# Kernel optimization log

Measured on AMD Instinct MI355X. Metric: run time of the kernel, lower is better.

Reference implementation:

```python
import jax, jax.numpy as jnp
from jax import lax
import numpy as np

B, T, I, H, L, O = 256, 200, 32, 512, 2, 7
EPS = 1e-12


def setup_inputs() -> dict:
    key = jax.random.key(0)
    ks = jax.random.split(key, 11)
    s = 0.05
    return {
        "x": jax.random.normal(ks[0], (B, T, I), dtype=jnp.float32),
        "w_ih0": jax.random.normal(ks[1], (4 * H, I), dtype=jnp.float32) * s,
        "w_hh0": jax.random.normal(ks[2], (4 * H, H), dtype=jnp.float32) * s,
        "b_ih0": jax.random.normal(ks[3], (4 * H,), dtype=jnp.float32) * s,
        "b_hh0": jax.random.normal(ks[4], (4 * H,), dtype=jnp.float32) * s,
        "w_ih1": jax.random.normal(ks[5], (4 * H, H), dtype=jnp.float32) * s,
        "w_hh1": jax.random.normal(ks[6], (4 * H, H), dtype=jnp.float32) * s,
        "b_ih1": jax.random.normal(ks[7], (4 * H,), dtype=jnp.float32) * s,
        "b_hh1": jax.random.normal(ks[8], (4 * H,), dtype=jnp.float32) * s,
        "w_fc": jax.random.normal(ks[9], (O, H), dtype=jnp.float32) * s,
        "b_fc": jax.random.normal(ks[10], (O,), dtype=jnp.float32) * s,
    }


def _lstm_layer(x_tbi, w_ih, w_hh, b_ih, b_hh):
    # x_tbi: [T, B, in]; PyTorch gate order i, f, g, o
    b = b_ih + b_hh
    hdim = w_hh.shape[1]
    batch = x_tbi.shape[1]
    # precompute input projections for all timesteps (one big GEMM)
    xg = jnp.einsum('tbi,gi->tbg', x_tbi, w_ih) + b  # [T, B, 4H]

    def step(carry, xgt):
        h, c = carry
        g = xgt + h @ w_hh.T
        i, f, gg, o = jnp.split(g, 4, axis=-1)
        c = jax.nn.sigmoid(f) * c + jax.nn.sigmoid(i) * jnp.tanh(gg)
        h = jax.nn.sigmoid(o) * jnp.tanh(c)
        return (h, c), h

    h0 = jnp.zeros((batch, hdim), x_tbi.dtype)
    (_, _), hs = lax.scan(step, (h0, h0), xg)
    return hs  # [T, B, H]


def reference(x, w_ih0, w_hh0, b_ih0, b_hh0, w_ih1, w_hh1, b_ih1, b_hh1, w_fc, b_fc):
    xt = jnp.transpose(x, (1, 0, 2))  # [T, B, I]
    h1 = _lstm_layer(xt, w_ih0, w_hh0, b_ih0, b_hh0)
    h2 = _lstm_layer(h1, w_ih1, w_hh1, b_ih1, b_hh1)
    last = h2[-1]  # [B, H] = output[:, -1, :]
    y = last @ w_fc.T + b_fc  # [B, O]
    p = jax.nn.sigmoid(y[:, :3])
    rt = jnp.tanh(y[:, 3:])
    # F.normalize(p=2, dim=1, eps=1e-12)
    r = rt / jnp.maximum(jnp.linalg.norm(rt, axis=1, keepdims=True), EPS)
    return (p, r)
```

## Files before the change

### kernel.cpp

```cpp
#include <hip/hip_runtime.h>
#include <hip/hip_bf16.h>

#define TSEQ  200
#define BATCH 256
#define INDIM 32
#define HID   512
#define GATES 2048

typedef __bf16 bf16x8 __attribute__((ext_vector_type(8)));
typedef float  f32x4  __attribute__((ext_vector_type(4)));
typedef unsigned long long u64;

static constexpr size_t OFF_PW_IH0 = 0;
static constexpr size_t OFF_PW_HH0 = 0x20000;
static constexpr size_t OFF_PW_IH1 = 0x220000;
static constexpr size_t OFF_PW_HH1 = 0x420000;
static constexpr size_t OFF_B0     = 0x620000;
static constexpr size_t OFF_B1     = 0x622000;
static constexpr size_t OFF_H1     = 0x624000;
static constexpr size_t OFF_H2     = 0x724000;
static constexpr size_t OFF_CTR    = 0x7A4000;
static constexpr size_t OFF_H2P    = 0x7A6000;
static constexpr size_t ZERO_OFF   = OFF_H1;
static constexpr size_t ZERO_LEN   = OFF_H2P + 0x80000 - OFF_H1;

__device__ __forceinline__ float sigm(float v) { return 1.f / (1.f + __expf(-v)); }

__device__ __forceinline__ bf16x8 as_bf16x8(f32x4 v) {
    union { f32x4 f; bf16x8 b; } u; u.f = v; return u.b;
}

__device__ __forceinline__ bf16x8 load16_coh(const bf16x8* p) {
    bf16x8 v;
    asm volatile("global_load_dwordx4 %0, %1, off sc0 sc1"
                 : "=v"(v) : "v"(p) : "memory");
    return v;
}

__device__ __forceinline__ void store16_coh(void* p, u64 v0, u64 v1) {
    union { u64 u[2]; f32x4 f; } cv; cv.u[0] = v0; cv.u[1] = v1;
    asm volatile("global_store_dwordx4 %0, %1, off sc0 sc1"
                 :: "v"(p), "v"(cv.f) : "memory");
}

__device__ __forceinline__ unsigned load_flag_coh(const unsigned* p) {
    unsigned v;
    asm volatile("global_load_dword %0, %1, off sc0 sc1\n\t"
                 "s_waitcnt vmcnt(0)"
                 : "=v"(v) : "v"(p) : "memory");
    return v;
}

__global__ void pack_w(const float* __restrict__ W, __bf16* __restrict__ out, int ktlog2)
{
    int tid = blockIdx.x * 256 + threadIdx.x;
    int K = 32 << ktlog2;
    int j    = tid & 7;
    int lane = (tid >> 3) & 63;
    int rest = tid >> 9;
    int kt   = rest & ((1 << ktlog2) - 1);
    int r2   = rest >> ktlog2;
    int lnt  = r2 & 7;
    int bn   = r2 >> 3;
    int type = lnt >> 1, half = lnt & 1;
    int g    = type * 512 + bn * 32 + half * 16 + (lane & 15);
    int kcol = kt * 32 + (lane >> 4) * 8 + j;
    out[tid] = (__bf16)W[g * K + kcol];
}

__global__ void bias_comb(const float* __restrict__ a0, const float* __restrict__ a1,
                          const float* __restrict__ a2, const float* __restrict__ a3,
                          float* __restrict__ o0, float* __restrict__ o1)
{
    int tid = blockIdx.x * 256 + threadIdx.x;
    if (tid < GATES) { o0[tid] = a0[tid] + a1[tid]; o1[tid] = a2[tid] + a3[tid]; }
}

__global__ __launch_bounds__(256, 1) void lstm_persist(const float* __restrict__ x,
                                                       const float* __restrict__ wfc,
                                                       const float* __restrict__ bfc,
                                                       char* __restrict__ ws,
                                                       float* __restrict__ out)
{
    const int layer = blockIdx.x >> 7;
    const int lb    = blockIdx.x & 127;
    const int mtp   = lb >> 4;
    const int bn    = lb & 15;
    const int wid   = threadIdx.x >> 6;
    const int half  = wid & 1;
    const int kh    = wid >> 1;
    const int lane  = threadIdx.x & 63;
    const int q     = lane >> 4;
    const int c16   = lane & 15;
    unsigned* flg   = (unsigned*)(ws + OFF_CTR) + (size_t)mtp * 64;

    __shared__ float  red[2][64][33];
    __shared__ __bf16 htr[1024];

    const float* bias = (const float*)(ws + (layer ? OFF_B1 : OFF_B0));
    const int hidx = bn * 32 + half * 16 + c16;
    const float bi  = bias[hidx];
    const float bff = bias[512 + hidx];
    const float bg  = bias[1024 + hidx];
    const float bo  = bias[1536 + hidx];

    const bf16x8* __restrict__ pBx = (const bf16x8*)(ws + OFF_PW_IH0);
    const bf16x8* __restrict__ pBh = (const bf16x8*)(ws + OFF_PW_HH0);
    const bf16x8* __restrict__ pB1 = (const bf16x8*)(ws + OFF_PW_IH1);
    const bf16x8* __restrict__ pB2 = (const bf16x8*)(ws + OFF_PW_HH1);
    float* __restrict__ h2p = (float*)(ws + OFF_H2P);

    f32x4 Bw[64];
    f32x4 Bx[4];
    if (layer == 0) {
        #pragma unroll
        for (int j = 0; j < 8; ++j)
            #pragma unroll
            for (int ty = 0; ty < 4; ++ty)
                Bw[j * 4 + ty] = *(const f32x4*)&pBh[((bn * 8 + ty * 2 + half) * 16 + kh * 8 + j) * 64 + lane];
        #pragma unroll
        for (int ty = 0; ty < 4; ++ty)
            Bx[ty] = *(const f32x4*)&pBx[(bn * 8 + ty * 2 + half) * 64 + lane];
    } else {
        const bf16x8* __restrict__ pW = kh ? pB2 : pB1;
        #pragma unroll
        for (int j = 0; j < 16; ++j)
            #pragma unroll
            for (int ty = 0; ty < 4; ++ty)
                Bw[j * 4 + ty] = *(const f32x4*)&pW[((bn * 8 + ty * 2 + half) * 16 + j) * 64 + lane];
    }

    float creg[8] = {0.f,0.f,0.f,0.f,0.f,0.f,0.f,0.f};

    auto loadA = [&](bf16x8* dst, const bf16x8* pA, int kt0) {
        #pragma unroll
        for (int j = 0; j < 8; ++j) {
            dst[j]     = load16_coh(&pA[((mtp * 2 + 0) * 16 + kt0 + j) * 64 + lane]);
            dst[8 + j] = load16_coh(&pA[((mtp * 2 + 1) * 16 + kt0 + j) * 64 + lane]);
        }
    };

    for (int k = 0; k <= TSEQ; ++k) {
        const bool active = layer ? (k >= 1) : (k < TSEQ);
        if (active) {
            const int t = k - layer;
            f32x4 acc[2][4] = {};

            const size_t h1rd = OFF_H1 + (size_t)((k + 3) & 3) * 0x40000;

            if (layer == 0) {
                const bf16x8* __restrict__ pA = (const bf16x8*)(ws + h1rd);
                bf16x8 af[16];
                loadA(af, pA, kh * 8);
                bf16x8 ax[2];
                if (kh == 0) {
                    #pragma unroll
                    for (int m = 0; m < 2; ++m) {
                        const int b = (mtp * 2 + m) * 16 + c16;
                        const float* xp = x + ((size_t)b * TSEQ + t) * INDIM + q * 8;
                        float4 xlo = *(const float4*)xp;
                        float4 xhi = *(const float4*)(xp + 4);
                        ax[m][0] = (__bf16)xlo.x; ax[m][1] = (__bf16)xlo.y;
                        ax[m][2] = (__bf16)xlo.z; ax[m][3] = (__bf16)xlo.w;
                        ax[m][4] = (__bf16)xhi.x; ax[m][5] = (__bf16)xhi.y;
                        ax[m][6] = (__bf16)xhi.z; ax[m][7] = (__bf16)xhi.w;
                    }
                }
                asm volatile("s_waitcnt vmcnt(0)" ::: "memory");
                __builtin_amdgcn_sched_barrier(0);
                if (kh == 0) {
                    #pragma unroll
                    for (int m = 0; m < 2; ++m)
                        #pragma unroll
                        for (int ty = 0; ty < 4; ++ty)
                            acc[m][ty] = __builtin_amdgcn_mfma_f32_16x16x32_bf16(ax[m], as_bf16x8(Bx[ty]), acc[m][ty], 0, 0, 0);
                }
                #pragma unroll
                for (int j = 0; j < 8; ++j) {
                    #pragma unroll
                    for (int ty = 0; ty < 4; ++ty) {
                        acc[0][ty] = __builtin_amdgcn_mfma_f32_16x16x32_bf16(af[j],     as_bf16x8(Bw[j * 4 + ty]), acc[0][ty], 0, 0, 0);
                        acc[1][ty] = __builtin_amdgcn_mfma_f32_16x16x32_bf16(af[8 + j], as_bf16x8(Bw[j * 4 + ty]), acc[1][ty], 0, 0, 0);
                    }
                }
            } else {
                const bf16x8* __restrict__ pA = kh
                    ? (const bf16x8*)(ws + OFF_H2 + (size_t)((k + 1) & 1) * 0x40000)
                    : (const bf16x8*)(ws + h1rd);
                bf16x8 a0[16], a1[16];
                loadA(a0, pA, 0);
                loadA(a1, pA, 8);
                asm volatile("s_waitcnt vmcnt(0)" ::: "memory");
                __builtin_amdgcn_sched_barrier(0);
                #pragma unroll
                for (int j = 0; j < 8; ++j) {
                    #pragma unroll
                    for (int ty = 0; ty < 4; ++ty) {
                        acc[0][ty] = __builtin_amdgcn_mfma_f32_16x16x32_bf16(a0[j],     as_bf16x8(Bw[j * 4 + ty]), acc[0][ty], 0, 0, 0);
                        acc[1][ty] = __builtin_amdgcn_mfma_f32_16x16x32_bf16(a0[8 + j], as_bf16x8(Bw[j * 4 + ty]), acc[1][ty], 0, 0, 0);
                    }
                }
                #pragma unroll
                for (int j = 0; j < 8; ++j) {
                    #pragma unroll
                    for (int ty = 0; ty < 4; ++ty) {
                        acc[0][ty] = __builtin_amdgcn_mfma_f32_16x16x32_bf16(a1[j],     as_bf16x8(Bw[(8 + j) * 4 + ty]), acc[0][ty], 0, 0, 0);
                        acc[1][ty] = __builtin_amdgcn_mfma_f32_16x16x32_bf16(a1[8 + j], as_bf16x8(Bw[(8 + j) * 4 + ty]), acc[1][ty], 0, 0, 0);
                    }
                }
            }

            if (kh == 1) {
                #pragma unroll
                for (int m = 0; m < 2; ++m)
                    #pragma unroll
                    for (int ty = 0; ty < 4; ++ty)
                        #pragma unroll
                        for (int r = 0; r < 4; ++r)
                            red[half][lane][m * 16 + ty * 4 + r] = acc[m][ty][r];
            }
            __syncthreads();

            if (kh == 0) {
                __bf16* __restrict__ hout = (__bf16*)(ws + (layer
                    ? OFF_H2 + (size_t)(k & 1) * 0x40000
                    : OFF_H1 + (size_t)(k & 3) * 0x40000));
                #pragma unroll
                for (int m = 0; m < 2; ++m) {
                    #pragma unroll
                    for (int r = 0; r < 4; ++r) {
                        float pi = acc[m][0][r] + red[half][lane][m * 16 + r]      + bi;
                        float pf = acc[m][1][r] + red[half][lane][m * 16 + 4 + r]  + bff;
                        float pg = acc[m][2][r] + red[half][lane][m * 16 + 8 + r]  + bg;
                        float po = acc[m][3][r] + red[half][lane][m * 16 + 12 + r] + bo;
                        float cn = sigm(pf) * creg[m * 4 + r] + sigm(pi) * tanhf(pg);
                        float hn = sigm(po) * tanhf(cn);
                        creg[m * 4 + r] = cn;
                        htr[half * 512 + (m * 16 + q * 4 + r) * 16 + c16] = (__bf16)hn;
                        if (layer == 1 && k == TSEQ) {
                            const int b = (mtp * 2 + m) * 16 + q * 4 + r;
                            __hip_atomic_store(&h2p[b * HID + hidx], hn,
                                               __ATOMIC_RELAXED, __HIP_MEMORY_SCOPE_AGENT);
                        }
                    }
                }
                const int bt   = lane >> 5;
                const int qa1  = (lane >> 4) & 1;
                const int b15r = lane & 15;
                const u64* lp = (const u64*)&htr[half * 512 + (bt * 16 + b15r) * 16 + qa1 * 8];
                u64 v0 = lp[0], v1 = lp[1];
                const int f = (((mtp * 2 + bt) * 16) + bn) * 64 + (half * 2 + qa1) * 16 + b15r;
                u64* gp = (u64*)hout + (size_t)f * 2;
                store16_coh(gp, v0, v1);
            }
        }

        asm volatile("s_waitcnt vmcnt(0)" ::: "memory");
        __syncthreads();
        if (threadIdx.x == 0)
            __hip_atomic_store(flg + layer * 16 + bn, (unsigned)(k + 1),
                               __ATOMIC_RELAXED, __HIP_MEMORY_SCOPE_AGENT);
        if (threadIdx.x < 32) {
            const int need = (layer == 0 && threadIdx.x >= 16 && k < TSEQ) ? (k - 1) : (k + 1);
            while ((int)load_flag_coh(flg + threadIdx.x) < need)
                __builtin_amdgcn_s_sleep(1);
        }
        __syncthreads();
    }

    if (threadIdx.x < 64) {
        const int b = mtp * 32 + layer * 16 + bn;
        const float* h = h2p + b * HID;
        float hv[8];
        #pragma unroll
        for (int j = 0; j < 8; ++j)
            hv[j] = __hip_atomic_load(&h[lane * 8 + j], __ATOMIC_RELAXED, __HIP_MEMORY_SCOPE_AGENT);
        float y[7];
        #pragma unroll
        for (int o = 0; o < 7; ++o) {
            const float* wrow = wfc + o * HID;
            float s = 0.f;
            #pragma unroll
            for (int j = 0; j < 8; ++j) s += hv[j] * wrow[lane * 8 + j];
            #pragma unroll
            for (int off = 32; off >= 1; off >>= 1) s += __shfl_down(s, off);
            y[o] = s;
        }
        if (lane == 0) {
            out[b * 3 + 0] = sigm(y[0] + bfc[0]);
            out[b * 3 + 1] = sigm(y[1] + bfc[1]);
            out[b * 3 + 2] = sigm(y[2] + bfc[2]);
            float r0 = tanhf(y[3] + bfc[3]);
            float r1 = tanhf(y[4] + bfc[4]);
            float r2 = tanhf(y[5] + bfc[5]);
            float r3 = tanhf(y[6] + bfc[6]);
            float n = sqrtf(r0 * r0 + r1 * r1 + r2 * r2 + r3 * r3);
            n = fmaxf(n, 1e-12f);
            out[768 + b * 4 + 0] = r0 / n;
            out[768 + b * 4 + 1] = r1 / n;
            out[768 + b * 4 + 2] = r2 / n;
            out[768 + b * 4 + 3] = r3 / n;
        }
    }
}

extern "C" void kernel_launch(void* const* d_in, const int* in_sizes, int n_in,
                              void* d_out, int out_size, void* d_ws, size_t ws_size,
                              hipStream_t stream)
{
    const float* x    = (const float*)d_in[0];
    const float* wih0 = (const float*)d_in[1];
    const float* whh0 = (const float*)d_in[2];
    const float* bih0 = (const float*)d_in[3];
    const float* bhh0 = (const float*)d_in[4];
    const float* wih1 = (const float*)d_in[5];
    const float* whh1 = (const float*)d_in[6];
    const float* bih1 = (const float*)d_in[7];
    const float* bhh1 = (const float*)d_in[8];
    const float* wfc  = (const float*)d_in[9];
    const float* bfc  = (const float*)d_in[10];
    char* ws = (char*)d_ws;

    hipMemsetAsync(ws + ZERO_OFF, 0, ZERO_LEN, stream);

    pack_w<<<256,  256, 0, stream>>>(wih0, (__bf16*)(ws + OFF_PW_IH0), 0);
    pack_w<<<4096, 256, 0, stream>>>(whh0, (__bf16*)(ws + OFF_PW_HH0), 4);
    pack_w<<<4096, 256, 0, stream>>>(wih1, (__bf16*)(ws + OFF_PW_IH1), 4);
    pack_w<<<4096, 256, 0, stream>>>(whh1, (__bf16*)(ws + OFF_PW_HH1), 4);
    bias_comb<<<8, 256, 0, stream>>>(bih0, bhh0, bih1, bhh1,
                                     (float*)(ws + OFF_B0), (float*)(ws + OFF_B1));

    lstm_persist<<<256, 256, 0, stream>>>(x, wfc, bfc, ws, (float*)d_out);
}
```

Baseline: 1.563 ms.

## Share h-state loads across wave pair via LDS staging and use fast tanh

Each wave pair now splits the per-step global loads of the recurrent h operand, with each wave fetching half. The halves are exchanged through a shared-memory staging buffer and a block barrier, which cuts the coherent global traffic on the serial recurrence path. tanhf is also replaced with an exp-based approximation in the gate and output activations. The trade-off is an extra __syncthreads per step plus LDS writes and reads, more shared memory per block, and slightly different tanh accuracy.

```diff
diff --git a/kernel.cpp b/kernel.cpp
--- a/kernel.cpp
+++ b/kernel.cpp
@@ -25,6 +25,12 @@
 static constexpr size_t ZERO_LEN   = OFF_H2P + 0x80000 - OFF_H1;
 
 __device__ __forceinline__ float sigm(float v) { return 1.f / (1.f + __expf(-v)); }
+
+__device__ __forceinline__ float tanh_fast(float v) {
+    float e = __expf(-2.0f * fabsf(v));
+    float t = (1.0f - e) / (1.0f + e);
+    return copysignf(t, v);
+}
 
 __device__ __forceinline__ bf16x8 as_bf16x8(f32x4 v) {
     union { f32x4 f; bf16x8 b; } u; u.f = v; return u.b;
@@ -96,6 +102,7 @@
 
     __shared__ float  red[2][64][33];
     __shared__ __bf16 htr[1024];
+    __shared__ bf16x8 stg[2][2][16][64];
 
     const float* bias = (const float*)(ws + (layer ? OFF_B1 : OFF_B0));
     const int hidx = bn * 32 + half * 16 + c16;
@@ -132,14 +139,6 @@
 
     float creg[8] = {0.f,0.f,0.f,0.f,0.f,0.f,0.f,0.f};
 
-    auto loadA = [&](bf16x8* dst, const bf16x8* pA, int kt0) {
-        #pragma unroll
-        for (int j = 0; j < 8; ++j) {
-            dst[j]     = load16_coh(&pA[((mtp * 2 + 0) * 16 + kt0 + j) * 64 + lane]);
-            dst[8 + j] = load16_coh(&pA[((mtp * 2 + 1) * 16 + kt0 + j) * 64 + lane]);
-        }
-    };
-
     for (int k = 0; k <= TSEQ; ++k) {
         const bool active = layer ? (k >= 1) : (k < TSEQ);
         if (active) {
@@ -150,8 +149,10 @@
 
             if (layer == 0) {
                 const bf16x8* __restrict__ pA = (const bf16x8*)(ws + h1rd);
-                bf16x8 af[16];
-                loadA(af, pA, kh * 8);
+                bf16x8 tmp0[8];
+                #pragma unroll
+                for (int j = 0; j < 8; ++j)
+                    tmp0[j] = load16_coh(&pA[((mtp * 2 + half) * 16 + kh * 8 + j) * 64 + lane]);
                 bf16x8 ax[2];
                 if (kh == 0) {
                     #pragma unroll
@@ -168,6 +169,16 @@
                 }
                 asm volatile("s_waitcnt vmcnt(0)" ::: "memory");
                 __builtin_amdgcn_sched_barrier(0);
+                #pragma unroll
+                for (int j = 0; j < 8; ++j)
+                    stg[kh][half][j][lane] = tmp0[j];
+                __syncthreads();
+                bf16x8 af[16];
+                #pragma unroll
+                for (int j = 0; j < 8; ++j) {
+                    af[j]     = stg[kh][0][j][lane];
+                    af[8 + j] = stg[kh][1][j][lane];
+                }
                 if (kh == 0) {
                     #pragma unroll
                     for (int m = 0; m < 2; ++m)
@@ -187,11 +198,24 @@
                 const bf16x8* __restrict__ pA = kh
                     ? (const bf16x8*)(ws + OFF_H2 + (size_t)((k + 1) & 1) * 0x40000)
                     : (const bf16x8*)(ws + h1rd);
-                bf16x8 a0[16], a1[16];
-                loadA(a0, pA, 0);
-                loadA(a1, pA, 8);
+                bf16x8 tmp[16];
+                #pragma unroll
+                for (int j = 0; j < 16; ++j)
+                    tmp[j] = load16_coh(&pA[((mtp * 2 + half) * 16 + j) * 64 + lane]);
                 asm volatile("s_waitcnt vmcnt(0)" ::: "memory");
                 __builtin_amdgcn_sched_barrier(0);
+                #pragma unroll
+                for (int j = 0; j < 16; ++j)
+                    stg[kh][half][j][lane] = tmp[j];
+                __syncthreads();
+                bf16x8 a0[16], a1[16];
+                #pragma unroll
+                for (int j = 0; j < 8; ++j) {
+                    a0[j]     = stg[kh][0][j][lane];
+                    a0[8 + j] = stg[kh][1][j][lane];
+                    a1[j]     = stg[kh][0][8 + j][lane];
+                    a1[8 + j] = stg[kh][1][8 + j][lane];
+                }
                 #pragma unroll
                 for (int j = 0; j < 8; ++j) {
                     #pragma unroll
@@ -233,8 +257,8 @@
                         float pf = acc[m][1][r] + red[half][lane][m * 16 + 4 + r]  + bff;
                         float pg = acc[m][2][r] + red[half][lane][m * 16 + 8 + r]  + bg;
                         float po = acc[m][3][r] + red[half][lane][m * 16 + 12 + r] + bo;
-                        float cn = sigm(pf) * creg[m * 4 + r] + sigm(pi) * tanhf(pg);
-                        float hn = sigm(po) * tanhf(cn);
+                        float cn = sigm(pf) * creg[m * 4 + r] + sigm(pi) * tanh_fast(pg);
+                        float hn = sigm(po) * tanh_fast(cn);
                         creg[m * 4 + r] = cn;
                         htr[half * 512 + (m * 16 + q * 4 + r) * 16 + c16] = (__bf16)hn;
                         if (layer == 1 && k == TSEQ) {
@@ -290,10 +314,10 @@
             out[b * 3 + 0] = sigm(y[0] + bfc[0]);
             out[b * 3 + 1] = sigm(y[1] + bfc[1]);
             out[b * 3 + 2] = sigm(y[2] + bfc[2]);
-            float r0 = tanhf(y[3] + bfc[3]);
-            float r1 = tanhf(y[4] + bfc[4]);
-            float r2 = tanhf(y[5] + bfc[5]);
-            float r3 = tanhf(y[6] + bfc[6]);
+            float r0 = tanh_fast(y[3] + bfc[3]);
+            float r1 = tanh_fast(y[4] + bfc[4]);
+            float r2 = tanh_fast(y[5] + bfc[5]);
+            float r3 = tanh_fast(y[6] + bfc[6]);
             float n = sqrtf(r0 * r0 + r1 * r1 + r2 * r2 + r3 * r3);
             n = fmaxf(n, 1e-12f);
             out[768 + b * 4 + 0] = r0 / n;
```

Result: faster. 1.433 ms (-8.4%).
